# Optimization experiments

Measured on AMD Instinct MI355X. Metric: run time of the kernel, lower is better.

## Reference

```python
import jax, jax.numpy as jnp
import numpy as np

NUM_HEADS = 16
SLICE_SIZE = 1024
SCALING = SLICE_SIZE ** 0.5  # module divides by sqrt(slice_size), as written


def setup_inputs() -> dict:
    key = jax.random.key(0)
    ks = jax.random.split(key, 9)
    B, S, D = 4, 2048, SLICE_SIZE
    sc = 0.02
    return {
        "x": jax.random.normal(ks[0], (B, S, D), dtype=jnp.float32),
        "Wq": jax.random.normal(ks[1], (D, D), dtype=jnp.float32) * sc,
        "bq": jax.random.normal(ks[2], (D,), dtype=jnp.float32) * sc,
        "Wk": jax.random.normal(ks[3], (D, D), dtype=jnp.float32) * sc,
        "bk": jax.random.normal(ks[4], (D,), dtype=jnp.float32) * sc,
        "Wv": jax.random.normal(ks[5], (D, D), dtype=jnp.float32) * sc,
        "bv": jax.random.normal(ks[6], (D,), dtype=jnp.float32) * sc,
        "Wp": jax.random.normal(ks[7], (D, D), dtype=jnp.float32) * sc,
        "bp": jax.random.normal(ks[8], (D,), dtype=jnp.float32) * sc,
    }


def _split_heads(t):
    # 'b s (h o) -> b h s o'
    b, s, d = t.shape
    return t.reshape(b, s, NUM_HEADS, d // NUM_HEADS).transpose(0, 2, 1, 3)


def reference(x, Wq, bq, Wk, bk, Wv, bv, Wp, bp):
    q = _split_heads(x @ Wq.T + bq)  # [B,H,S,O]
    k = _split_heads(x @ Wk.T + bk)
    v = _split_heads(x @ Wv.T + bv)
    energy = jnp.einsum('bhqo,bhko->bhqk', q, k)  # full score matrix
    attn = jax.nn.softmax(energy / SCALING, axis=-1)
    # Faithful to source: 'b h q k, b h v o -> b h v o' sums attn over (q,k)
    out = jnp.einsum('bhqk,bhvo->bhvo', attn, v)
    b, h, s, o = out.shape
    out = out.transpose(0, 2, 1, 3).reshape(b, s, h * o)  # 'b h v o -> b v (h o)'
    return out @ Wp.T + bp
```

## Files before the change

### kernel.cpp

```cpp
#include <hip/hip_runtime.h>
#include <cstdint>


typedef unsigned short u16;
typedef __bf16 bf16x8 __attribute__((ext_vector_type(8)));
typedef float f32x4 __attribute__((ext_vector_type(4)));

__device__ __forceinline__ u16 f2bf(float f) {
  unsigned int u = __float_as_uint(f);
  u += 0x7fffu + ((u >> 16) & 1u);
  return (u16)(u >> 16);
}

__device__ __forceinline__ bf16x8 cvt8(float4 a, float4 b) {
  bf16x8 r;
  r[0] = (__bf16)a.x; r[1] = (__bf16)a.y; r[2] = (__bf16)a.z; r[3] = (__bf16)a.w;
  r[4] = (__bf16)b.x; r[5] = (__bf16)b.y; r[6] = (__bf16)b.z; r[7] = (__bf16)b.w;
  return r;
}

__device__ __forceinline__ void load16(const void* g, void* l) {
  auto gp = (const __attribute__((address_space(1))) unsigned int*)(uintptr_t)g;
  auto lp = (__attribute__((address_space(3))) unsigned int*)(unsigned int)(uintptr_t)l;
  __builtin_amdgcn_global_load_lds(gp, lp, 16, 0, 0);
}

__global__ void k_prep(const float* __restrict__ Wv, const float* __restrict__ bv,
                       const float* __restrict__ Wp, const float* __restrict__ bp,
                       u16* __restrict__ wpb, u16* __restrict__ wvtb,
                       float* __restrict__ cv) {
  __shared__ float tile[32][33];
  const int b = blockIdx.x;
  const int tid = threadIdx.x;
  if (b < 1024) {
    const long base = (long)b * 1024 + tid * 4;
    const float4 v = *(const float4*)(Wp + base);
    ushort4 o;
    o.x = f2bf(v.x); o.y = f2bf(v.y); o.z = f2bf(v.z); o.w = f2bf(v.w);
    *(ushort4*)(wpb + base) = o;
  } else if (b < 2048) {
    const int tb = b - 1024;
    const int bi = (tb & 31) * 32;
    const int bj = (tb >> 5) * 32;
    const int tx = tid & 31;
    const int ty = tid >> 5;
    for (int r = ty; r < 32; r += 8)
      tile[r][tx] = Wv[(long)(bj + r) * 1024 + bi + tx];
    __syncthreads();
    for (int r = ty; r < 32; r += 8)
      wvtb[(long)(bi + r) * 1024 + bj + tx] = f2bf(tile[tx][r]);
  } else {
    const int row = (b - 2048) * 4 + (tid >> 6);
    const int lane = tid & 63;
    const float* w = Wp + (long)row * 1024;
    float s = 0.f;
    for (int j = lane; j < 1024; j += 64) s += w[j] * bv[j];
    for (int off = 32; off; off >>= 1) s += __shfl_down(s, off, 64);
    if (lane == 0) cv[row] = 2048.f * s + bp[row];
  }
}

template <int MODE>
__global__ __launch_bounds__(MODE == 0 ? 512 : 256) void k_gemm(
    const void* __restrict__ Ain, const u16* __restrict__ B, void* __restrict__ OutV,
    const float* __restrict__ bias, int M, int N, int K) {
  constexpr int BM = (MODE == 0) ? 128 : 64;
  constexpr int BN = (MODE == 0) ? 128 : 64;
  constexpr int T  = (MODE == 0) ? 512 : 256;
  constexpr int WTM = (MODE == 0) ? 64 : 32;
  constexpr int WTN = 32;
  constexpr int AccM = WTM / 16;
  constexpr int AccN = WTN / 16;

  __shared__ u16 As[2][BM * 64];
  __shared__ u16 Bs[2][BN * 64];

  const int tid = threadIdx.x;
  const int lane = tid & 63;
  const int wv = tid >> 6;
  const int waveM = (wv & 1) * WTM;
  const int waveN = (wv >> 1) * WTN;
  const int l15 = lane & 15;
  const int quad = lane >> 4;

  long bm, bn;
  if constexpr (MODE == 0) {
    const int id = blockIdx.x;
    const int xcd = id & 7;
    const int j = id >> 3;
    const int nb = N >> 7;
    const int mPerXcd = M / 128 / 8;
    bm = (long)(xcd * mPerXcd + j / nb) * 128;
    bn = (long)(j % nb) * 128;
  } else {
    bm = (long)(blockIdx.x >> 4) * 64;
    bn = (long)(blockIdx.x & 15) * 64;
  }

  const int nT = K >> 6;

  const int rl = tid >> 3;
  const int cs = (tid & 7) ^ (rl & 7);
  const u16* Bg0 = B + (bn + rl) * (long)K + cs * 8;
  constexpr int RPC = T / 8;

  const float* Afg = nullptr;
  const u16* Ag0 = nullptr;
  int ar = 0, as0 = 0, as1 = 0;
  if constexpr (MODE == 0) {
    const float* Af = (const float*)Ain;
    ar = tid >> 2;
    const int ap = tid & 3;
    Afg = Af + (bm + ar) * (long)K + ap * 16;
    as0 = ((2 * ap)     ^ (ar & 7)) * 8;
    as1 = ((2 * ap + 1) ^ (ar & 7)) * 8;
  } else {
    Ag0 = (const u16*)Ain + (bm + rl) * (long)K + cs * 8;
  }

  const f32x4 zero = {0.f, 0.f, 0.f, 0.f};
  f32x4 acc[AccM][AccN];
#pragma unroll
  for (int i = 0; i < AccM; ++i)
#pragma unroll
    for (int j = 0; j < AccN; ++j) acc[i][j] = zero;

  const int rq0 = quad ^ (l15 & 7);
  const int rq1 = (4 + quad) ^ (l15 & 7);

  if constexpr (MODE == 0) {
    const float4 v0 = *(const float4*)(Afg + 0);
    const float4 v1 = *(const float4*)(Afg + 4);
    const float4 v2 = *(const float4*)(Afg + 8);
    const float4 v3 = *(const float4*)(Afg + 12);
    u16* Bd = &Bs[0][0] + tid * 8;
    load16(Bg0, Bd);
    load16(Bg0 + (long)RPC * K, Bd + RPC * 64);
    u16* Aw = &As[0][0] + ar * 64;
    *(bf16x8*)(Aw + as0) = cvt8(v0, v1);
    *(bf16x8*)(Aw + as1) = cvt8(v2, v3);
  } else {
    u16* Ad = &As[0][0] + tid * 8;
    u16* Bd = &Bs[0][0] + tid * 8;
    load16(Ag0, Ad);
    load16(Ag0 + (long)RPC * K, Ad + RPC * 64);
    load16(Bg0, Bd);
    load16(Bg0 + (long)RPC * K, Bd + RPC * 64);
  }
  asm volatile("s_waitcnt vmcnt(0) lgkmcnt(0)" ::: "memory");
  __builtin_amdgcn_s_barrier();

  int cur = 0;
  for (int t = 0; t < nT; ++t) {
    const bool more = (t + 1) < nT;
    const long k1 = (long)(t + 1) << 6;

    float4 v0, v1, v2, v3;
    if (more) {
      if constexpr (MODE == 0) {
        const float* ag = Afg + k1;
        v0 = *(const float4*)(ag + 0);
        v1 = *(const float4*)(ag + 4);
        v2 = *(const float4*)(ag + 8);
        v3 = *(const float4*)(ag + 12);
        u16* Bd = &Bs[cur ^ 1][0] + tid * 8;
        load16(Bg0 + k1, Bd);
        load16(Bg0 + k1 + (long)RPC * K, Bd + RPC * 64);
      } else {
        u16* Ad = &As[cur ^ 1][0] + tid * 8;
        u16* Bd = &Bs[cur ^ 1][0] + tid * 8;
        load16(Ag0 + k1, Ad);
        load16(Ag0 + k1 + (long)RPC * K, Ad + RPC * 64);
        load16(Bg0 + k1, Bd);
        load16(Bg0 + k1 + (long)RPC * K, Bd + RPC * 64);
      }
    }
    __builtin_amdgcn_sched_barrier(0);

    const u16* Asb = &As[cur][0];
    const u16* Bsb = &Bs[cur][0];
    bf16x8 af[2][AccM], bg[2][AccN];
#pragma unroll
    for (int i = 0; i < AccM; ++i) {
      const int ra = (waveM + i * 16 + l15) * 64;
      af[0][i] = *(const bf16x8*)(Asb + ra + rq0 * 8);
      af[1][i] = *(const bf16x8*)(Asb + ra + rq1 * 8);
    }
#pragma unroll
    for (int j = 0; j < AccN; ++j) {
      const int rb = (waveN + j * 16 + l15) * 64;
      bg[0][j] = *(const bf16x8*)(Bsb + rb + rq0 * 8);
      bg[1][j] = *(const bf16x8*)(Bsb + rb + rq1 * 8);
    }
    asm volatile("s_waitcnt lgkmcnt(0)" ::: "memory");
    __builtin_amdgcn_sched_barrier(0);

#pragma unroll
    for (int kk = 0; kk < 2; ++kk)
#pragma unroll
      for (int i = 0; i < AccM; ++i)
#pragma unroll
        for (int j = 0; j < AccN; ++j)
          acc[i][j] = __builtin_amdgcn_mfma_f32_16x16x32_bf16(af[kk][i], bg[kk][j],
                                                              acc[i][j], 0, 0, 0);

    if (more) {
      if constexpr (MODE == 0) {
        u16* Aw = &As[cur ^ 1][0] + ar * 64;
        *(bf16x8*)(Aw + as0) = cvt8(v0, v1);
        *(bf16x8*)(Aw + as1) = cvt8(v2, v3);
      }
      asm volatile("s_waitcnt vmcnt(0) lgkmcnt(0)" ::: "memory");
      __builtin_amdgcn_s_barrier();
      cur ^= 1;
    }
  }

#pragma unroll
  for (int i = 0; i < AccM; ++i) {
    const long gm = bm + waveM + i * 16 + quad * 4;
#pragma unroll
    for (int j = 0; j < AccN; ++j) {
      const long gn = bn + waveN + j * 16 + l15;
      if constexpr (MODE == 0) {
        float* outp = (float*)OutV;
        const float bb = bias[gn];
#pragma unroll
        for (int r = 0; r < 4; ++r)
          outp[(gm + r) * N + gn] = acc[i][j][r] + bb;
      } else {
        u16* outp = (u16*)OutV;
#pragma unroll
        for (int r = 0; r < 4; ++r)
          outp[(gm + r) * N + gn] = f2bf(acc[i][j][r] * 2048.f);
      }
    }
  }
}

extern "C" void kernel_launch(void* const* d_in, const int* in_sizes, int n_in,
                              void* d_out, int out_size, void* d_ws, size_t ws_size,
                              hipStream_t stream) {
  const float* x  = (const float*)d_in[0];
  const float* Wv = (const float*)d_in[5];
  const float* bv = (const float*)d_in[6];
  const float* Wp = (const float*)d_in[7];
  const float* bp = (const float*)d_in[8];

  char* ws = (char*)d_ws;
  u16* wpb   = (u16*)(ws + (16u << 20));
  u16* wvtb  = (u16*)(ws + (18u << 20));
  u16* m2b   = (u16*)(ws + (20u << 20));
  float* cv  = (float*)(ws + (22u << 20));

  k_prep<<<2304, 256, 0, stream>>>(Wv, bv, Wp, bp, wpb, wvtb, cv);

  k_gemm<1><<<256, 256, 0, stream>>>(wpb, wvtb, m2b, nullptr, 1024, 1024, 1024);

  k_gemm<0><<<512, 512, 0, stream>>>(x, m2b, d_out, cv, 8192, 1024, 1024);
}
```

Measured before the change: 150.1 us.

## Prefetch fp32 A tiles two stages ahead in the main GEMM loop

The fp32 activation loads for the x GEMM are now issued two K-tiles ahead and held in registers. At the start of each iteration they are converted and written into LDS for the next stage, so global latency is hidden across a full iteration instead of being waited on before the barrier. Waitcnt now uses vmcnt(4) so the in-flight A prefetch is not drained at each barrier. This costs extra live registers and relies on the hand-counted vmcnt being correct.

```diff
diff --git a/kernel.cpp b/kernel.cpp
--- a/kernel.cpp
+++ b/kernel.cpp
@@ -128,17 +128,24 @@
   const int rq0 = quad ^ (l15 & 7);
   const int rq1 = (4 + quad) ^ (l15 & 7);
 
+  float4 va0, va1, va2, va3;
+
   if constexpr (MODE == 0) {
-    const float4 v0 = *(const float4*)(Afg + 0);
-    const float4 v1 = *(const float4*)(Afg + 4);
-    const float4 v2 = *(const float4*)(Afg + 8);
-    const float4 v3 = *(const float4*)(Afg + 12);
+    va0 = *(const float4*)(Afg + 0);
+    va1 = *(const float4*)(Afg + 4);
+    va2 = *(const float4*)(Afg + 8);
+    va3 = *(const float4*)(Afg + 12);
+    u16* Aw = &As[0][0] + ar * 64;
+    *(bf16x8*)(Aw + as0) = cvt8(va0, va1);
+    *(bf16x8*)(Aw + as1) = cvt8(va2, va3);
     u16* Bd = &Bs[0][0] + tid * 8;
     load16(Bg0, Bd);
     load16(Bg0 + (long)RPC * K, Bd + RPC * 64);
-    u16* Aw = &As[0][0] + ar * 64;
-    *(bf16x8*)(Aw + as0) = cvt8(v0, v1);
-    *(bf16x8*)(Aw + as1) = cvt8(v2, v3);
+    va0 = *(const float4*)(Afg + 64 + 0);
+    va1 = *(const float4*)(Afg + 64 + 4);
+    va2 = *(const float4*)(Afg + 64 + 8);
+    va3 = *(const float4*)(Afg + 64 + 12);
+    asm volatile("s_waitcnt vmcnt(4) lgkmcnt(0)" ::: "memory");
   } else {
     u16* Ad = &As[0][0] + tid * 8;
     u16* Bd = &Bs[0][0] + tid * 8;
@@ -146,27 +153,34 @@
     load16(Ag0 + (long)RPC * K, Ad + RPC * 64);
     load16(Bg0, Bd);
     load16(Bg0 + (long)RPC * K, Bd + RPC * 64);
-  }
-  asm volatile("s_waitcnt vmcnt(0) lgkmcnt(0)" ::: "memory");
+    asm volatile("s_waitcnt vmcnt(0)" ::: "memory");
+  }
   __builtin_amdgcn_s_barrier();
 
   int cur = 0;
   for (int t = 0; t < nT; ++t) {
-    const bool more = (t + 1) < nT;
+    const bool w1 = (t + 1) < nT;
+    const bool w2 = (t + 2) < nT;
     const long k1 = (long)(t + 1) << 6;
 
-    float4 v0, v1, v2, v3;
-    if (more) {
-      if constexpr (MODE == 0) {
-        const float* ag = Afg + k1;
-        v0 = *(const float4*)(ag + 0);
-        v1 = *(const float4*)(ag + 4);
-        v2 = *(const float4*)(ag + 8);
-        v3 = *(const float4*)(ag + 12);
+    if constexpr (MODE == 0) {
+      if (w1) {
+        u16* Aw = &As[cur ^ 1][0] + ar * 64;
+        *(bf16x8*)(Aw + as0) = cvt8(va0, va1);
+        *(bf16x8*)(Aw + as1) = cvt8(va2, va3);
         u16* Bd = &Bs[cur ^ 1][0] + tid * 8;
         load16(Bg0 + k1, Bd);
         load16(Bg0 + k1 + (long)RPC * K, Bd + RPC * 64);
-      } else {
+      }
+      if (w2) {
+        const float* ag = Afg + ((long)(t + 2) << 6);
+        va0 = *(const float4*)(ag + 0);
+        va1 = *(const float4*)(ag + 4);
+        va2 = *(const float4*)(ag + 8);
+        va3 = *(const float4*)(ag + 12);
+      }
+    } else {
+      if (w1) {
         u16* Ad = &As[cur ^ 1][0] + tid * 8;
         u16* Bd = &Bs[cur ^ 1][0] + tid * 8;
         load16(Ag0 + k1, Ad);
@@ -204,13 +218,16 @@
           acc[i][j] = __builtin_amdgcn_mfma_f32_16x16x32_bf16(af[kk][i], bg[kk][j],
                                                               acc[i][j], 0, 0, 0);
 
-    if (more) {
+    if (w1) {
       if constexpr (MODE == 0) {
-        u16* Aw = &As[cur ^ 1][0] + ar * 64;
-        *(bf16x8*)(Aw + as0) = cvt8(v0, v1);
-        *(bf16x8*)(Aw + as1) = cvt8(v2, v3);
-      }
-      asm volatile("s_waitcnt vmcnt(0) lgkmcnt(0)" ::: "memory");
+        if (w2) {
+          asm volatile("s_waitcnt vmcnt(4)" ::: "memory");
+        } else {
+          asm volatile("s_waitcnt vmcnt(0)" ::: "memory");
+        }
+      } else {
+        asm volatile("s_waitcnt vmcnt(0)" ::: "memory");
+      }
       __builtin_amdgcn_s_barrier();
       cur ^= 1;
     }
```

Measured after the change: 148.7 us. No clear change (-0.9%).
